# Kernel tuning notes

Measured on AMD Instinct MI355X. Metric: run time of the kernel, lower is better.

## Reference

```python
import jax, jax.numpy as jnp
import numpy as np

NUM_HEADS = 128
NUM_QK_BITS = 8
NUM_V_BITS = 8


def setup_inputs() -> dict:
    key = jax.random.key(0)
    ks = jax.random.split(key, 8)
    B, S, D = 2, 4096, 1024
    HQ = NUM_HEADS * NUM_QK_BITS  # 1024
    HV = NUM_HEADS * NUM_V_BITS   # 1024
    sc = 0.02
    return {
        "hidden_states": jax.random.normal(ks[0], (B, S, D), dtype=jnp.float32),
        "Wq": jax.random.normal(ks[1], (HQ, D), dtype=jnp.float32) * sc,
        "Wk": jax.random.normal(ks[2], (HQ, D), dtype=jnp.float32) * sc,
        "Wv": jax.random.normal(ks[3], (HV, D), dtype=jnp.float32) * sc,
        "Wo": jax.random.normal(ks[4], (D, HV), dtype=jnp.float32) * sc,
        "emb0": jax.random.normal(ks[5], (HV,), dtype=jnp.float32) * sc,
        "emb1": jax.random.normal(ks[6], (HV,), dtype=jnp.float32) * sc,
        "suffix_window": 8,
    }


def _rosa_forward(hidden_states, Wq, Wk, Wv, Wo, emb0, emb1, W):
    B, S, D = hidden_states.shape
    H, BQ, BV = NUM_HEADS, NUM_QK_BITS, NUM_V_BITS

    # projections -> [B, H, S, bits]
    q = (hidden_states @ Wq.T).reshape(B, S, H, BQ).transpose(0, 2, 1, 3)
    k = (hidden_states @ Wk.T).reshape(B, S, H, BQ).transpose(0, 2, 1, 3)
    v = (hidden_states @ Wv.T).reshape(B, S, H, BV).transpose(0, 2, 1, 3)

    # soft bits in [0, 1] (differentiable relaxation of bit quantization)
    qb = jax.nn.sigmoid(q)
    kb = jax.nn.sigmoid(k)
    vb = jax.nn.sigmoid(v)

    # causal suffix window: key/value at position t-d for offset d in [0, W)
    def shift(x, d):  # x: [B,H,S,C] -> x[t-d], front-padded with zeros
        return jnp.pad(x, ((0, 0), (0, 0), (d, 0), (0, 0)))[:, :, :S, :]

    kw = jnp.stack([shift(kb, d) for d in range(W)], axis=3)  # [B,H,S,W,BQ]
    vw = jnp.stack([shift(vb, d) for d in range(W)], axis=3)  # [B,H,S,W,BV]

    # Hamming-style agreement: sum_b [qb*kb + (1-qb)*(1-kb)]
    dot = jnp.einsum("bhsc,bhswc->bhsw", qb, kw)
    qsum = jnp.sum(qb, axis=-1)[..., None]        # [B,H,S,1]
    ksum = jnp.sum(kw, axis=-1)                   # [B,H,S,W]
    agree = BQ + 2.0 * dot - qsum - ksum          # [B,H,S,W]

    scale = 1.0 / jnp.sqrt(jnp.float32(BQ))
    scores = agree * scale

    # valid only when t - d >= 0
    valid = jnp.arange(S)[:, None] >= jnp.arange(W)[None, :]  # [S,W]
    scores = jnp.where(valid[None, None], scores, jnp.float32(-1e30))
    weights = jax.nn.softmax(scores, axis=-1)

    out = jnp.einsum("bhsw,bhswc->bhsc", weights, vw)  # [B,H,S,BV]
    out = out.transpose(0, 2, 1, 3).reshape(B, S, H * BV)

    # interpolation gate then output projection
    out = emb1 * out + emb0 * (1.0 - out)
    return out @ Wo.T


def reference(hidden_states, Wq, Wk, Wv, Wo, emb0, emb1, suffix_window):
    return _rosa_forward(hidden_states, Wq, Wk, Wv, Wo, emb0, emb1, suffix_window)
```

## Files before the change

kernel.cpp:

```cpp
#include <hip/hip_runtime.h>
#include <hip/hip_bf16.h>

typedef __bf16 bf16;
typedef __bf16 bf16x8 __attribute__((ext_vector_type(8)));
typedef int i32x4 __attribute__((ext_vector_type(4)));
typedef signed char scx8 __attribute__((ext_vector_type(8)));

__device__ __forceinline__ void gload_lds16(const void* g, void* l) {
  __builtin_amdgcn_global_load_lds(
      (const __attribute__((address_space(1))) void*)g,
      (__attribute__((address_space(3))) void*)l, 16, 0, 0);
}

template <int K>
__global__ __launch_bounds__(256, 3) void gemm_qkv(
    const signed char* __restrict__ A, const signed char* __restrict__ Bw,
    const float* __restrict__ sA, const float* __restrict__ sB,
    bf16* __restrict__ C, int M, int N) {
  __shared__ __align__(16) char smem[49152];
  const int tid = threadIdx.x;
  const int lane = tid & 63;
  const int wave = tid >> 6;

  const int nb = N >> 7;
  const int nwg = gridDim.x;
  const int q8 = nwg >> 3;
  const int tile = ((int)blockIdx.x & 7) * q8 + ((int)blockIdx.x >> 3);
  const int m0 = (tile / nb) << 7;
  const int n0 = (tile % nb) << 7;

  const int wm = (wave >> 1) << 6;
  const int wn = (wave & 1) << 6;

  i32x4 acc[4][4] = {};

  const int r_in = lane >> 2;
  const int swz = ((lane >> 3) & 3) << 4;
  const int scolb = ((lane & 3) << 4) ^ swz;
  const signed char* gA0 = A + (size_t)(m0 + (wave << 4) + r_in) * K + scolb;
  const signed char* gA1 = gA0 + ((size_t)K << 6);
  const signed char* gB0 = Bw + (size_t)(n0 + (wave << 4) + r_in) * K + scolb;
  const signed char* gB1 = gB0 + ((size_t)K << 6);
  const int ldsoff = (wave << 10) + (lane << 4);

  constexpr int NT = K >> 6;

  auto stage = [&](int t) {
    char* b = smem + (t % 3) * 16384 + ldsoff;
    const int ko = t << 6;
    gload_lds16(gA0 + ko, b);
    gload_lds16(gA1 + ko, b + 4096);
    gload_lds16(gB0 + ko, b + 8192);
    gload_lds16(gB1 + ko, b + 12288);
  };

  const int lrow = lane & 15;
  const int koff = ((lane >> 4) << 4) ^ (((lrow >> 1) & 3) << 4);
  const int aoff = (wm + lrow) * 64 + koff;
  const int boff = 8192 + (wn + lrow) * 64 + koff;

  stage(0);
  stage(1);

#pragma unroll
  for (int t = 0; t < NT; ++t) {
    if (t == NT - 1) {
      asm volatile("s_waitcnt vmcnt(0)" ::: "memory");
    } else {
      asm volatile("s_waitcnt vmcnt(4)" ::: "memory");
    }
    __builtin_amdgcn_s_barrier();
    __builtin_amdgcn_sched_barrier(0);

    i32x4 af[4], bg[4];
    const char* base = smem + (t % 3) * 16384;
#pragma unroll
    for (int i = 0; i < 4; ++i) {
      af[i] = *(const i32x4*)(base + aoff + (i << 10));
      bg[i] = *(const i32x4*)(base + boff + (i << 10));
    }

    if (t + 2 < NT) stage(t + 2);

#pragma unroll
    for (int i = 0; i < 4; ++i)
#pragma unroll
      for (int j = 0; j < 4; ++j)
        acc[i][j] =
            __builtin_amdgcn_mfma_i32_16x16x64_i8(af[i], bg[j], acc[i][j], 0, 0, 0);
  }

  const int col0 = n0 + wn + lrow;
  const int rowb = m0 + wm + ((lane >> 4) << 2);
  float sb[4];
#pragma unroll
  for (int j = 0; j < 4; ++j) sb[j] = sB[col0 + (j << 4)];
#pragma unroll
  for (int i = 0; i < 4; ++i)
#pragma unroll
    for (int r = 0; r < 4; ++r) {
      const int row = rowb + (i << 4) + r;
      const float sa = sA[row];
#pragma unroll
      for (int j = 0; j < 4; ++j) {
        const size_t idx = (size_t)row * N + (col0 + (j << 4));
        const float v = (float)acc[i][j][r] * (sa * sb[j]);
        C[idx] = (bf16)(1.0f / (1.0f + __expf(-v)));
      }
    }
}

template <int K>
__global__ __launch_bounds__(256, 4) void gemm_out(
    const signed char* __restrict__ A, const signed char* __restrict__ Bw,
    const float* __restrict__ sB, const float* __restrict__ bias,
    float* __restrict__ C, int M, int N) {
  __shared__ __align__(16) char smem[36864];
  const int tid = threadIdx.x;
  const int lane = tid & 63;
  const int wave = tid >> 6;

  const int nb = N >> 7;
  const int nwg = gridDim.x;
  const int q8 = nwg >> 3;
  const int tile = ((int)blockIdx.x & 7) * q8 + ((int)blockIdx.x >> 3);
  const int m0 = (tile / nb) << 6;
  const int n0 = (tile % nb) << 7;

  const int wm = (wave >> 1) << 5;
  const int wn = (wave & 1) << 6;

  i32x4 acc[2][4] = {};

  const int r_in = lane >> 2;
  const int swz = ((lane >> 3) & 3) << 4;
  const int scolb = ((lane & 3) << 4) ^ swz;
  const signed char* gA0 = A + (size_t)(m0 + (wave << 4) + r_in) * K + scolb;
  const signed char* gB0 = Bw + (size_t)(n0 + (wave << 4) + r_in) * K + scolb;
  const signed char* gB1 = gB0 + ((size_t)K << 6);
  const int ldsoff = (wave << 10) + (lane << 4);

  constexpr int NT = K >> 6;

  auto stage = [&](int t) {
    char* b = smem + (t % 3) * 12288 + ldsoff;
    const int ko = t << 6;
    gload_lds16(gA0 + ko, b);
    gload_lds16(gB0 + ko, b + 4096);
    gload_lds16(gB1 + ko, b + 8192);
  };

  const int lrow = lane & 15;
  const int koff = ((lane >> 4) << 4) ^ (((lrow >> 1) & 3) << 4);
  const int aoff = (wm + lrow) * 64 + koff;
  const int boff = 4096 + (wn + lrow) * 64 + koff;

  stage(0);
  stage(1);

#pragma unroll
  for (int t = 0; t < NT; ++t) {
    if (t == NT - 1) {
      asm volatile("s_waitcnt vmcnt(0)" ::: "memory");
    } else {
      asm volatile("s_waitcnt vmcnt(3)" ::: "memory");
    }
    __builtin_amdgcn_s_barrier();
    __builtin_amdgcn_sched_barrier(0);

    i32x4 af[2], bg[4];
    const char* base = smem + (t % 3) * 12288;
#pragma unroll
    for (int i = 0; i < 2; ++i)
      af[i] = *(const i32x4*)(base + aoff + (i << 10));
#pragma unroll
    for (int j = 0; j < 4; ++j)
      bg[j] = *(const i32x4*)(base + boff + (j << 10));

    if (t + 2 < NT) stage(t + 2);

#pragma unroll
    for (int i = 0; i < 2; ++i)
#pragma unroll
      for (int j = 0; j < 4; ++j)
        acc[i][j] =
            __builtin_amdgcn_mfma_i32_16x16x64_i8(af[i], bg[j], acc[i][j], 0, 0, 0);
  }

  const int col0 = n0 + wn + lrow;
  const int rowb = m0 + wm + ((lane >> 4) << 2);
  float sb[4], bi[4];
#pragma unroll
  for (int j = 0; j < 4; ++j) {
    sb[j] = sB[col0 + (j << 4)] * (1.0f / 127.0f);
    bi[j] = bias[col0 + (j << 4)];
  }
#pragma unroll
  for (int i = 0; i < 2; ++i)
#pragma unroll
    for (int r = 0; r < 4; ++r) {
      const int row = rowb + (i << 4) + r;
#pragma unroll
      for (int j = 0; j < 4; ++j) {
        const size_t idx = (size_t)row * N + (col0 + (j << 4));
        C[idx] = (float)acc[i][j][r] * sb[j] + bi[j];
      }
    }
}

__global__ __launch_bounds__(256) void rosa_attn(
    const bf16* __restrict__ qkv, signed char* __restrict__ Oq) {
  const int t = blockIdx.x * 256 + threadIdx.x;
  const int row = t >> 7;
  const int h = t & 127;
  const int sp = row & 4095;

  const bf16* qptr = qkv + (size_t)row * 3072 + h * 8;
  bf16x8 qv = *(const bf16x8*)qptr;
  float qb[8], qsum = 0.f;
#pragma unroll
  for (int c = 0; c < 8; ++c) {
    qb[c] = (float)qv[c];
    qsum += qb[c];
  }

  float oacc[8] = {};
  float wsum = 0.f;
  const int wmax = (sp + 1 < 8) ? (sp + 1) : 8;
  const float scale = 0.35355339059327373f;

  for (int d = 0; d < wmax; ++d) {
    const bf16* base = qkv + (size_t)(row - d) * 3072 + h * 8;
    bf16x8 kv = *(const bf16x8*)(base + 1024);
    bf16x8 vv = *(const bf16x8*)(base + 2048);
    float dot = 0.f, ksum = 0.f;
#pragma unroll
    for (int c = 0; c < 8; ++c) {
      const float kb = (float)kv[c];
      dot += qb[c] * kb;
      ksum += kb;
    }
    const float score = (8.0f + 2.0f * dot - qsum - ksum) * scale;
    const float w = __expf(score);
    wsum += w;
#pragma unroll
    for (int c = 0; c < 8; ++c) oacc[c] += w * (float)vv[c];
  }

  const float inv = 127.0f / wsum;
  scx8 outv;
#pragma unroll
  for (int c = 0; c < 8; ++c)
    outv[c] = (signed char)(int)(oacc[c] * inv + 0.5f);
  *(scx8*)(Oq + (size_t)row * 1024 + h * 8) = outv;
}

__global__ __launch_bounds__(256) void quant_all(
    const float* __restrict__ X, const float* __restrict__ Wq,
    const float* __restrict__ Wk, const float* __restrict__ Wv,
    const float* __restrict__ Wo, const float* __restrict__ emb0,
    const float* __restrict__ emb1, signed char* __restrict__ Xq,
    signed char* __restrict__ Wqkvq, signed char* __restrict__ W2q,
    float* __restrict__ sx, float* __restrict__ sw, float* __restrict__ sw2,
    float* __restrict__ bias) {
  const int wrow = (blockIdx.x << 2) + ((threadIdx.x) >> 6);
  const int lane = threadIdx.x & 63;
  const float* srow;
  signed char* drow;
  float* sc;
  bool isW2 = false;
  int w2r = 0;
  if (wrow < 8192) {
    srow = X + (size_t)wrow * 1024; drow = Xq + (size_t)wrow * 1024;
    sc = sx + wrow;
  } else if (wrow < 11264) {
    const int r = wrow - 8192;
    const float* w = (r < 1024) ? Wq : (r < 2048 ? Wk : Wv);
    srow = w + (size_t)(r & 1023) * 1024;
    drow = Wqkvq + (size_t)r * 1024; sc = sw + r;
  } else {
    const int r = wrow - 11264; w2r = r;
    srow = Wo + (size_t)r * 1024; drow = W2q + (size_t)r * 1024; sc = sw2 + r;
    isW2 = true;
  }
  float4 v[4];
  float bsum = 0.f, m = 0.f;
#pragma unroll
  for (int p = 0; p < 4; ++p) {
    v[p] = ((const float4*)srow)[lane + (p << 6)];
    if (isW2) {
      const float4 e1 = ((const float4*)emb1)[lane + (p << 6)];
      const float4 e0 = ((const float4*)emb0)[lane + (p << 6)];
      bsum += v[p].x * e0.x + v[p].y * e0.y + v[p].z * e0.z + v[p].w * e0.w;
      v[p].x *= (e1.x - e0.x); v[p].y *= (e1.y - e0.y);
      v[p].z *= (e1.z - e0.z); v[p].w *= (e1.w - e0.w);
    }
    m = fmaxf(m, fmaxf(fmaxf(fabsf(v[p].x), fabsf(v[p].y)),
                       fmaxf(fabsf(v[p].z), fabsf(v[p].w))));
  }
#pragma unroll
  for (int off = 32; off; off >>= 1) m = fmaxf(m, __shfl_xor(m, off));
  if (isW2) {
#pragma unroll
    for (int off = 32; off; off >>= 1) bsum += __shfl_xor(bsum, off);
  }
  const float inv = (m > 0.f) ? 127.f / m : 0.f;
#pragma unroll
  for (int p = 0; p < 4; ++p) {
    const int q0 = __float2int_rn(v[p].x * inv) & 255;
    const int q1 = __float2int_rn(v[p].y * inv) & 255;
    const int q2 = __float2int_rn(v[p].z * inv) & 255;
    const int q3 = __float2int_rn(v[p].w * inv) & 255;
    ((int*)drow)[lane + (p << 6)] = q0 | (q1 << 8) | (q2 << 16) | (q3 << 24);
  }
  if (lane == 0) {
    *sc = (m > 0.f) ? m / 127.f : 0.f;
    if (isW2) bias[w2r] = bsum;
  }
}

extern "C" void kernel_launch(void* const* d_in, const int* in_sizes, int n_in,
                              void* d_out, int out_size, void* d_ws,
                              size_t ws_size, hipStream_t stream) {
  const float* X = (const float*)d_in[0];
  const float* Wq = (const float*)d_in[1];
  const float* Wk = (const float*)d_in[2];
  const float* Wv = (const float*)d_in[3];
  const float* Wo = (const float*)d_in[4];
  const float* emb0 = (const float*)d_in[5];
  const float* emb1 = (const float*)d_in[6];

  char* ws = (char*)d_ws;
  signed char* Xq    = (signed char*)(ws + 0);
  signed char* Wqkvq = (signed char*)(ws + 8388608);
  signed char* W2q   = (signed char*)(ws + 11534336);
  float* sx   = (float*)(ws + 12582912);
  float* sw   = (float*)(ws + 12615680);
  float* sw2  = (float*)(ws + 12627968);
  float* bias = (float*)(ws + 12632064);
  bf16* QKVb  = (bf16*)(ws + 16777216);
  signed char* Oq = (signed char*)(ws + 67108864);
  float* out = (float*)d_out;

  quant_all<<<3072, 256, 0, stream>>>(X, Wq, Wk, Wv, Wo, emb0, emb1, Xq,
                                      Wqkvq, W2q, sx, sw, sw2, bias);

  gemm_qkv<1024><<<1536, 256, 0, stream>>>(Xq, Wqkvq, sx, sw, QKVb, 8192, 3072);

  rosa_attn<<<4096, 256, 0, stream>>>(QKVb, Oq);

  gemm_out<1024><<<1024, 256, 0, stream>>>(Oq, W2q, sw2, bias, out, 8192, 1024);
}
```

Measured before the change: 97.82 us.

## Reuse K/V across 8 consecutive rows per thread in rosa attention; runtime-K QKV GEMM

Each rosa_attn thread now handles 8 consecutive sequence rows for one head and keeps a rolling register window of K/V vectors and their sums. Each K/V row is loaded about twice instead of eight times. The grid shrinks from 4096 to 512 blocks, trading less memory traffic for fewer threads in flight. Separately, gemm_qkv takes K as a runtime argument with a non-unrolled loop and pointer increments, which may slightly change codegen for the main GEMM.

Result: faster. 88.99 us, median of 2 (-9.0%).

```diff
diff --git a/kernel.cpp b/kernel.cpp
--- a/kernel.cpp
+++ b/kernel.cpp
@@ -12,11 +12,10 @@
       (__attribute__((address_space(3))) void*)l, 16, 0, 0);
 }
 
-template <int K>
 __global__ __launch_bounds__(256, 3) void gemm_qkv(
     const signed char* __restrict__ A, const signed char* __restrict__ Bw,
     const float* __restrict__ sA, const float* __restrict__ sB,
-    bf16* __restrict__ C, int M, int N) {
+    bf16* __restrict__ C, int M, int N, int K) {
   __shared__ __align__(16) char smem[49152];
   const int tid = threadIdx.x;
   const int lane = tid & 63;
@@ -43,28 +42,26 @@
   const signed char* gB1 = gB0 + ((size_t)K << 6);
   const int ldsoff = (wave << 10) + (lane << 4);
 
-  constexpr int NT = K >> 6;
-
-  auto stage = [&](int t) {
-    char* b = smem + (t % 3) * 16384 + ldsoff;
-    const int ko = t << 6;
-    gload_lds16(gA0 + ko, b);
-    gload_lds16(gA1 + ko, b + 4096);
-    gload_lds16(gB0 + ko, b + 8192);
-    gload_lds16(gB1 + ko, b + 12288);
+  auto stage = [&](int buf) {
+    char* b = smem + buf * 16384 + ldsoff;
+    gload_lds16(gA0, b);
+    gload_lds16(gA1, b + 4096);
+    gload_lds16(gB0, b + 8192);
+    gload_lds16(gB1, b + 12288);
+    gA0 += 64; gA1 += 64; gB0 += 64; gB1 += 64;
   };
 
   const int lrow = lane & 15;
   const int koff = ((lane >> 4) << 4) ^ (((lrow >> 1) & 3) << 4);
-  const int aoff = (wm + lrow) * 64 + koff;
-  const int boff = 8192 + (wn + lrow) * 64 + koff;
+
+  const int nt = K >> 6;
 
   stage(0);
   stage(1);
 
-#pragma unroll
-  for (int t = 0; t < NT; ++t) {
-    if (t == NT - 1) {
+  int buf = 0, pb = 2;
+  for (int t = 0; t < nt; ++t) {
+    if (t == nt - 1) {
       asm volatile("s_waitcnt vmcnt(0)" ::: "memory");
     } else {
       asm volatile("s_waitcnt vmcnt(4)" ::: "memory");
@@ -73,14 +70,14 @@
     __builtin_amdgcn_sched_barrier(0);
 
     i32x4 af[4], bg[4];
-    const char* base = smem + (t % 3) * 16384;
+    const char* base = smem + buf * 16384;
 #pragma unroll
     for (int i = 0; i < 4; ++i) {
-      af[i] = *(const i32x4*)(base + aoff + (i << 10));
-      bg[i] = *(const i32x4*)(base + boff + (i << 10));
-    }
-
-    if (t + 2 < NT) stage(t + 2);
+      af[i] = *(const i32x4*)(base + (wm + (i << 4) + lrow) * 64 + koff);
+      bg[i] = *(const i32x4*)(base + 8192 + (wn + (i << 4) + lrow) * 64 + koff);
+    }
+
+    if (t + 2 < nt) stage(pb);
 
 #pragma unroll
     for (int i = 0; i < 4; ++i)
@@ -88,6 +85,9 @@
       for (int j = 0; j < 4; ++j)
         acc[i][j] =
             __builtin_amdgcn_mfma_i32_16x16x64_i8(af[i], bg[j], acc[i][j], 0, 0, 0);
+
+    if (++buf == 3) buf = 0;
+    if (++pb == 3) pb = 0;
   }
 
   const int col0 = n0 + wn + lrow;
@@ -211,48 +211,71 @@
 __global__ __launch_bounds__(256) void rosa_attn(
     const bf16* __restrict__ qkv, signed char* __restrict__ Oq) {
   const int t = blockIdx.x * 256 + threadIdx.x;
-  const int row = t >> 7;
   const int h = t & 127;
-  const int sp = row & 4095;
-
-  const bf16* qptr = qkv + (size_t)row * 3072 + h * 8;
-  bf16x8 qv = *(const bf16x8*)qptr;
-  float qb[8], qsum = 0.f;
-#pragma unroll
-  for (int c = 0; c < 8; ++c) {
-    qb[c] = (float)qv[c];
-    qsum += qb[c];
-  }
-
-  float oacc[8] = {};
-  float wsum = 0.f;
-  const int wmax = (sp + 1 < 8) ? (sp + 1) : 8;
+  const int rbase = (t >> 7) << 3;
+  const int hoff = h * 8;
   const float scale = 0.35355339059327373f;
 
-  for (int d = 0; d < wmax; ++d) {
-    const bf16* base = qkv + (size_t)(row - d) * 3072 + h * 8;
-    bf16x8 kv = *(const bf16x8*)(base + 1024);
-    bf16x8 vv = *(const bf16x8*)(base + 2048);
-    float dot = 0.f, ksum = 0.f;
+  bf16x8 kr[8], vr[8];
+  float ksum[8];
+
+  if ((rbase & 4095) != 0) {
+#pragma unroll
+    for (int p = 1; p <= 7; ++p) {
+      const int row = rbase - p;
+      const int slot = (8 - p) & 7;
+      const bf16* base = qkv + (size_t)row * 3072 + hoff;
+      kr[slot] = *(const bf16x8*)(base + 1024);
+      vr[slot] = *(const bf16x8*)(base + 2048);
+      float s = 0.f;
+#pragma unroll
+      for (int c = 0; c < 8; ++c) s += (float)kr[slot][c];
+      ksum[slot] = s;
+    }
+  }
+
+#pragma unroll
+  for (int rr = 0; rr < 8; ++rr) {
+    const int row = rbase + rr;
+    const int sp = row & 4095;
+    const bf16* base = qkv + (size_t)row * 3072 + hoff;
+    bf16x8 qv = *(const bf16x8*)base;
+    kr[rr] = *(const bf16x8*)(base + 1024);
+    vr[rr] = *(const bf16x8*)(base + 2048);
+    float qb[8], qsum = 0.f, s = 0.f;
 #pragma unroll
     for (int c = 0; c < 8; ++c) {
-      const float kb = (float)kv[c];
-      dot += qb[c] * kb;
-      ksum += kb;
-    }
-    const float score = (8.0f + 2.0f * dot - qsum - ksum) * scale;
-    const float w = __expf(score);
-    wsum += w;
-#pragma unroll
-    for (int c = 0; c < 8; ++c) oacc[c] += w * (float)vv[c];
-  }
-
-  const float inv = 127.0f / wsum;
-  scx8 outv;
-#pragma unroll
-  for (int c = 0; c < 8; ++c)
-    outv[c] = (signed char)(int)(oacc[c] * inv + 0.5f);
-  *(scx8*)(Oq + (size_t)row * 1024 + h * 8) = outv;
+      qb[c] = (float)qv[c];
+      qsum += qb[c];
+      s += (float)kr[rr][c];
+    }
+    ksum[rr] = s;
+
+    const int wmax = (sp + 1 < 8) ? (sp + 1) : 8;
+    float oacc[8] = {};
+    float wsum = 0.f;
+#pragma unroll
+    for (int d = 0; d < 8; ++d) {
+      if (d < wmax) {
+        const int slot = (rr - d) & 7;
+        float dot = 0.f;
+#pragma unroll
+        for (int c = 0; c < 8; ++c) dot += qb[c] * (float)kr[slot][c];
+        const float score = (8.0f + 2.0f * dot - qsum - ksum[slot]) * scale;
+        const float w = __expf(score);
+        wsum += w;
+#pragma unroll
+        for (int c = 0; c < 8; ++c) oacc[c] += w * (float)vr[slot][c];
+      }
+    }
+
+    const float inv = 127.0f / wsum;
+    scx8 outv;
+#pragma unroll
+    for (int c = 0; c < 8; ++c)
+      outv[c] = (signed char)(int)(oacc[c] * inv + 0.5f);
+    *(scx8*)(Oq + (size_t)row * 1024 + hoff) = outv;
+  }
 }
 
 __global__ __launch_bounds__(256) void quant_all(
@@ -345,9 +368,9 @@
   quant_all<<<3072, 256, 0, stream>>>(X, Wq, Wk, Wv, Wo, emb0, emb1, Xq,
                                       Wqkvq, W2q, sx, sw, sw2, bias);
 
-  gemm_qkv<1024><<<1536, 256, 0, stream>>>(Xq, Wqkvq, sx, sw, QKVb, 8192, 3072);
-
-  rosa_attn<<<4096, 256, 0, stream>>>(QKVb, Oq);
+  gemm_qkv<<<1536, 256, 0, stream>>>(Xq, Wqkvq, sx, sw, QKVb, 8192, 3072, 1024);
+
+  rosa_attn<<<512, 256, 0, stream>>>(QKVb, Oq);
 
   gemm_out<1024><<<1024, 256, 0, stream>>>(Oq, W2q, sw2, bias, out, 8192, 1024);
 }
```
